# Performance work log

Measured on AMD Instinct MI355X. Metric: run time of the kernel, lower is better.

The kernel has to match this reference:

```python
import jax, jax.numpy as jnp
import numpy as np

N, E, HID, H, L, EF = 50000, 640000, 128, 8, 3, 16
C = HID // H  # 16, per-head output channels (concat=True)
NEG_SLOPE = 0.2
LN_EPS = 1e-5


def setup_inputs() -> dict:
    key = jax.random.key(0)
    ks = jax.random.split(key, 12)
    s = 0.05
    x = jax.random.normal(ks[0], (N, HID), jnp.float32)
    batch_index = jnp.sort(jax.random.randint(ks[1], (N,), 0, 64, dtype=jnp.int32))
    edge_index = jax.random.randint(ks[2], (2, E), 0, N, dtype=jnp.int32)
    edge_attr = jax.random.normal(ks[3], (E, EF), jnp.float32)
    # edge_transform: Linear(EF, HID)
    Wt = jax.random.normal(ks[4], (EF, HID), jnp.float32) * s
    bt = jnp.zeros((HID,), jnp.float32)
    # per-layer GATv2 params (stacked over L layers)
    Wl = jax.random.normal(ks[5], (L, HID, HID), jnp.float32) * s  # lin_l (source)
    bl = jnp.zeros((L, HID), jnp.float32)
    Wr = jax.random.normal(ks[6], (L, HID, HID), jnp.float32) * s  # lin_r (target)
    br = jnp.zeros((L, HID), jnp.float32)
    We = jax.random.normal(ks[7], (L, HID, HID), jnp.float32) * s  # lin_edge (no bias)
    att = jax.random.normal(ks[8], (L, H, C), jnp.float32) * s
    bias_o = jnp.zeros((L, HID), jnp.float32)
    ln_g = jnp.ones((L, HID), jnp.float32)
    ln_b = jnp.zeros((L, HID), jnp.float32)
    return dict(x=x, batch_index=batch_index, edge_index=edge_index, edge_attr=edge_attr,
                Wt=Wt, bt=bt, Wl=Wl, bl=bl, Wr=Wr, br=br, We=We, att=att,
                bias_o=bias_o, ln_g=ln_g, ln_b=ln_b)


def _layer_norm(x, g, b):
    mu = jnp.mean(x, axis=-1, keepdims=True)
    var = jnp.var(x, axis=-1, keepdims=True)
    return g * (x - mu) * jax.lax.rsqrt(var + LN_EPS) + b


def _gatv2_layer(x, ea, src, dst, Wl, bl, Wr, br, We, att, bias_o):
    # node transforms: lin_l for source features, lin_r for target features
    xl = (x @ Wl + bl).reshape(N, H, C)
    xr = (x @ Wr + br).reshape(N, H, C)
    em = (ea @ We).reshape(E, H, C)
    # per-edge attention logits (GATv2: leaky_relu AFTER the sum, then dot with att)
    m = jax.nn.leaky_relu(xl[src] + xr[dst] + em, NEG_SLOPE)  # [E,H,C]
    logits = jnp.einsum('ehc,hc->eh', m, att)                  # [E,H]
    # segment softmax over incoming edges of each destination node
    lmax = jax.ops.segment_max(logits, dst, num_segments=N)    # [N,H]
    p = jnp.exp(logits - lmax[dst])
    denom = jax.ops.segment_sum(p, dst, num_segments=N)        # [N,H]
    alpha = p / (denom[dst] + 1e-16)
    # weighted scatter-aggregate of source messages
    out = jax.ops.segment_sum(xl[src] * alpha[:, :, None], dst, num_segments=N)  # [N,H,C]
    return out.reshape(N, HID) + bias_o


def reference(x, batch_index, edge_index, edge_attr, Wt, bt, Wl, bl, Wr, br, We, att, bias_o, ln_g, ln_b):
    src, dst = edge_index[0], edge_index[1]
    ea = edge_attr @ Wt + bt  # shared edge_transform, [E,HID]
    for l in range(L):
        out = _gatv2_layer(x, ea, src, dst, Wl[l], bl[l], Wr[l], br[l], We[l], att[l], bias_o[l])
        out = _layer_norm(out, ln_g[l], ln_b[l])
        x = jax.nn.relu(out) + x  # dropout p=0 -> identity; residual
    return x
```

## Files before the change

kernel.cpp:

```cpp
#include <hip/hip_runtime.h>

#define N_NODES 50000
#define N_EDGES 640000
#define HID 128
#define EF 16
#define NLAYERS 3
#define CHUNK 32
#define SCAN_BLOCKS 196

typedef __attribute__((ext_vector_type(8))) short short8;
typedef __attribute__((ext_vector_type(4))) float f32x4;
typedef __attribute__((ext_vector_type(2))) float f32x2;

__device__ __forceinline__ unsigned short f2bf(float f) {
  unsigned int u = __float_as_uint(f);
  u = u + 0x7FFFu + ((u >> 16) & 1u);
  return (unsigned short)(u >> 16);
}

__device__ __forceinline__ float dpp_hadd8(float v) {
  int x;
  x = __builtin_amdgcn_update_dpp(0, __float_as_int(v), 0xB1, 0xF, 0xF, true);
  v += __int_as_float(x);
  x = __builtin_amdgcn_update_dpp(0, __float_as_int(v), 0x4E, 0xF, 0xF, true);
  v += __int_as_float(x);
  x = __builtin_amdgcn_update_dpp(0, __float_as_int(v), 0x141, 0xF, 0xF, true);
  v += __int_as_float(x);
  return v;
}

__device__ __forceinline__ int pslot(int j) {
  return (((j >> 4) * 8 + (j & 7)) << 1) + ((j >> 3) & 1);
}

__global__ __launch_bounds__(256) void k_prep(const float* __restrict__ Wt,
                                              const float* __restrict__ bt,
                                              const float* __restrict__ We,
                                              float* __restrict__ Mt,
                                              float* __restrict__ ct) {
  int id = blockIdx.x * 256 + threadIdx.x;
  const int total = NLAYERS * (EF + 1) * HID;
  if (id >= total) return;
  int l = id / ((EF + 1) * HID);
  int r = id % ((EF + 1) * HID);
  int row = r / HID;
  int j = r % HID;
  const float* Wel = We + l * HID * HID;
  float s = 0.f;
  if (row < EF) {
    const float* wtr = Wt + row * HID;
    for (int i = 0; i < HID; ++i) s += wtr[i] * Wel[i * HID + j];
    Mt[(l * EF + row) * HID + pslot(j)] = s;
  } else {
    for (int i = 0; i < HID; ++i) s += bt[i] * Wel[i * HID + j];
    ct[l * HID + pslot(j)] = s;
  }
}

__global__ __launch_bounds__(256) void k_cvtx(const float* __restrict__ x,
                                              unsigned short* __restrict__ xbf) {
  int id = blockIdx.x * 256 + threadIdx.x;
  const int total = N_NODES * HID / 8;
  if (id >= total) return;
  const float4* p = (const float4*)(x + id * 8);
  float4 a = p[0], b = p[1];
  unsigned short o[8] = {f2bf(a.x), f2bf(a.y), f2bf(a.z), f2bf(a.w),
                         f2bf(b.x), f2bf(b.y), f2bf(b.z), f2bf(b.w)};
  *(uint4*)(xbf + id * 8) = *(uint4*)o;
}

__global__ __launch_bounds__(256) void k_cvtw(const float* __restrict__ Wl,
                                              const float* __restrict__ Wr,
                                              unsigned short* __restrict__ WT) {
  int id = blockIdx.x * 256 + threadIdx.x;
  const int total = NLAYERS * 2 * HID * HID;
  if (id >= total) return;
  int k = id & (HID - 1);
  int n = (id >> 7) & (HID - 1);
  int s = (id >> 14) & 1;
  int l = id >> 15;
  const float* W = (s == 0 ? Wl : Wr) + (size_t)l * HID * HID;
  WT[id] = f2bf(W[k * HID + n]);
}

__global__ __launch_bounds__(256) void k_zero(int* __restrict__ counts, int* __restrict__ fill) {
  int id = blockIdx.x * 256 + threadIdx.x;
  if (id < N_NODES) { counts[id] = 0; fill[id] = 0; }
}

__global__ __launch_bounds__(256) void k_hist(const int* __restrict__ dst, int* __restrict__ counts) {
  int e = blockIdx.x * 256 + threadIdx.x;
  if (e < N_EDGES) atomicAdd(&counts[dst[e]], 1);
}

__global__ __launch_bounds__(256) void k_scan1(const int* __restrict__ counts,
                                               int* __restrict__ rowptr,
                                               int* __restrict__ bsum) {
  __shared__ int sc[256];
  int t = threadIdx.x;
  int i = blockIdx.x * 256 + t;
  int v = (i < N_NODES) ? counts[i] : 0;
  sc[t] = v;
  __syncthreads();
  for (int off = 1; off < 256; off <<= 1) {
    int u = 0;
    if (t >= off) u = sc[t - off];
    __syncthreads();
    sc[t] += u;
    __syncthreads();
  }
  if (i < N_NODES) rowptr[i] = sc[t] - v;
  if (t == 255) bsum[blockIdx.x] = sc[255];
}

__global__ __launch_bounds__(256) void k_scan2(int* __restrict__ bsum) {
  __shared__ int sc[256];
  int t = threadIdx.x;
  int v = (t < SCAN_BLOCKS) ? bsum[t] : 0;
  sc[t] = v;
  __syncthreads();
  for (int off = 1; off < 256; off <<= 1) {
    int u = 0;
    if (t >= off) u = sc[t - off];
    __syncthreads();
    sc[t] += u;
    __syncthreads();
  }
  bsum[t] = sc[t] - v;
}

__global__ __launch_bounds__(256) void k_scan3(int* __restrict__ rowptr, const int* __restrict__ bsum) {
  int t = threadIdx.x;
  int i = blockIdx.x * 256 + t;
  if (i < N_NODES) rowptr[i] += bsum[blockIdx.x];
  if (i == 0) rowptr[N_NODES] = N_EDGES;
}

__global__ __launch_bounds__(256) void k_fill(const int* __restrict__ src,
                                              const int* __restrict__ dst,
                                              const int* __restrict__ rowptr,
                                              int* __restrict__ fill,
                                              int* __restrict__ ssrc,
                                              const float* __restrict__ eattr,
                                              float* __restrict__ easrt) {
  int e = blockIdx.x * 256 + threadIdx.x;
  if (e >= N_EDGES) return;
  int d = dst[e];
  int pos = atomicAdd(&fill[d], 1);
  int idx = rowptr[d] + pos;
  ssrc[idx] = src[e];
  const float4* pe = (const float4*)(eattr + (size_t)e * EF);
  float4* po = (float4*)(easrt + (size_t)idx * EF);
#pragma unroll
  for (int q = 0; q < 4; ++q) po[q] = pe[q];
}

__global__ __launch_bounds__(256) void k_gemm_mfma(const unsigned short* __restrict__ xbf,
                                                   const unsigned short* __restrict__ WTl,
                                                   const float* __restrict__ bl,
                                                   const float* __restrict__ br,
                                                   const float* __restrict__ ctl,
                                                   unsigned short* __restrict__ xlb,
                                                   unsigned short* __restrict__ xrb) {
  __shared__ short As[64 * 136];
  __shared__ short Bs[128 * 136];
  int t = threadIdx.x;
  int s = blockIdx.y;
  int row0 = blockIdx.x * 64;

  const uint4* gx = (const uint4*)xbf;
#pragma unroll
  for (int p = 0; p < 4; ++p) {
    int c = t + p * 256;
    int row = c >> 4, col16 = c & 15;
    int grow = row0 + row;
    if (grow >= N_NODES) grow = N_NODES - 1;
    uint4 v = gx[grow * 16 + col16];
    *(uint4*)(&As[row * 136 + col16 * 8]) = v;
  }
  const uint4* gw = (const uint4*)WTl;
#pragma unroll
  for (int p = 0; p < 8; ++p) {
    int c = t + p * 256;
    int row = c >> 4, col16 = c & 15;
    uint4 v = gw[s * 2048 + row * 16 + col16];
    *(uint4*)(&Bs[row * 136 + col16 * 8]) = v;
  }
  __syncthreads();

  int lane = t & 63, w = t >> 6;
  int quad = lane >> 4, lm = lane & 15;
  f32x4 acc[4][2];
#pragma unroll
  for (int mf = 0; mf < 4; ++mf)
#pragma unroll
    for (int nf = 0; nf < 2; ++nf) acc[mf][nf] = (f32x4)(0.f);

#pragma unroll
  for (int ks = 0; ks < 4; ++ks) {
    short8 af[4], bf[2];
#pragma unroll
    for (int mf = 0; mf < 4; ++mf)
      af[mf] = *(short8*)(&As[(mf * 16 + lm) * 136 + ks * 32 + quad * 8]);
#pragma unroll
    for (int nf = 0; nf < 2; ++nf)
      bf[nf] = *(short8*)(&Bs[(w * 32 + nf * 16 + lm) * 136 + ks * 32 + quad * 8]);
#pragma unroll
    for (int mf = 0; mf < 4; ++mf)
#pragma unroll
      for (int nf = 0; nf < 2; ++nf)
        acc[mf][nf] = __builtin_amdgcn_mfma_f32_16x16x32_bf16(af[mf], bf[nf], acc[mf][nf], 0, 0, 0);
  }

  const float* bias = (s == 0) ? bl : br;
  unsigned short* out = (s == 0) ? xlb : xrb;
#pragma unroll
  for (int nf = 0; nf < 2; ++nf) {
    int n = w * 32 + nf * 16 + lm;
    int slot = pslot(n);
    float bv = bias[n] + ((s == 1) ? ctl[slot] : 0.f);
#pragma unroll
    for (int mf = 0; mf < 4; ++mf) {
#pragma unroll
      for (int r = 0; r < 4; ++r) {
        int grow = row0 + mf * 16 + quad * 4 + r;
        if (grow < N_NODES) out[(size_t)grow * HID + slot] = f2bf(acc[mf][nf][r] + bv);
      }
    }
  }
}

__global__ __launch_bounds__(64) void k_fused(const float* __restrict__ xin,
                                              const unsigned int* __restrict__ xlb,
                                              const unsigned int* __restrict__ xrb,
                                              const int* __restrict__ rowptr,
                                              const int* __restrict__ ssrc,
                                              const float* __restrict__ easrt,
                                              const float* __restrict__ Mt,
                                              const float* __restrict__ att,
                                              const float* __restrict__ bias_o,
                                              const float* __restrict__ lng,
                                              const float* __restrict__ lnb,
                                              float* __restrict__ xout,
                                              unsigned short* __restrict__ xbf_out) {
  __shared__ float ea_s[CHUNK][EF];
  __shared__ int src_s[CHUNK];
  int n = blockIdx.x;
  int l = threadIdx.x;
  int j0 = (l >> 3) * 16 + (l & 7), j1 = j0 + 8;

  f32x2 mtp[EF];
#pragma unroll
  for (int k = 0; k < EF; ++k) mtp[k] = *(const f32x2*)(&Mt[k * HID + l * 2]);
  unsigned int ur = xrb[(size_t)n * 64 + l];
  f32x2 base;
  base.x = __uint_as_float(ur << 16);
  base.y = __uint_as_float(ur & 0xFFFF0000u);
  f32x2 attp = {att[j0], att[j1]};
  int beg = rowptr[n], end = rowptr[n + 1];

  f32x2 acc = {0.f, 0.f};
  float denom = 0.f;

  for (int c0 = beg; c0 < end; c0 += CHUNK) {
    int cnt = min(CHUNK, end - c0);
    if (l < cnt) src_s[l] = ssrc[c0 + l];
    for (int q = l; q < cnt * 4; q += 64) {
      int i = q >> 2, part = q & 3;
      *(float4*)(&ea_s[i][part * 4]) =
          *(const float4*)(easrt + (size_t)(c0 + i) * EF + part * 4);
    }

    auto edge = [&](int i, unsigned int u) {
      f32x2 xls;
      xls.x = __uint_as_float(u << 16);
      xls.y = __uint_as_float(u & 0xFFFF0000u);
      f32x2 m = base + xls;
#pragma unroll
      for (int k = 0; k < EF; ++k) m += ea_s[i][k] * mtp[k];
      f32x2 am = {__int_as_float(__float_as_int(m.x) & 0x7FFFFFFF),
                  __int_as_float(__float_as_int(m.y) & 0x7FFFFFFF)};
      m = 0.6f * m + 0.4f * am;
      f32x2 v2 = m * attp;
      float vs = dpp_hadd8(v2.x + v2.y);
      float p = __expf(vs);
      denom += p;
      acc += xls * p;
    };

    unsigned int cur[4];
#pragma unroll
    for (int q = 0; q < 4; ++q)
      cur[q] = (q < cnt) ? xlb[(size_t)src_s[q] * 64 + l] : 0u;
    int cnt4 = cnt & ~3;
    for (int i = 0; i < cnt4; i += 4) {
      unsigned int nxt[4];
#pragma unroll
      for (int q = 0; q < 4; ++q) {
        int idx = i + 4 + q;
        nxt[q] = (idx < cnt) ? xlb[(size_t)src_s[idx] * 64 + l] : 0u;
      }
#pragma unroll
      for (int q = 0; q < 4; ++q) edge(i + q, cur[q]);
#pragma unroll
      for (int q = 0; q < 4; ++q) cur[q] = nxt[q];
    }
#pragma unroll
    for (int q = 0; q < 4; ++q)
      if (cnt4 + q < cnt) edge(cnt4 + q, cur[q]);
  }

  f32x2 outp;
  float inv = 1.f / (denom + 1e-16f);
  outp.x = acc.x * inv + bias_o[j0];
  outp.y = acc.y * inv + bias_o[j1];
  float s1 = outp.x + outp.y;
  float s2 = outp.x * outp.x + outp.y * outp.y;
#pragma unroll
  for (int mask = 1; mask <= 32; mask <<= 1) {
    s1 += __shfl_xor(s1, mask);
    s2 += __shfl_xor(s2, mask);
  }
  float mu = s1 * (1.f / 128.f);
  float var = s2 * (1.f / 128.f) - mu * mu;
  float rs = rsqrtf(var + 1e-5f);
  float y0 = lng[j0] * (outp.x - mu) * rs + lnb[j0];
  float y1 = lng[j1] * (outp.y - mu) * rs + lnb[j1];
  float r0 = fmaxf(y0, 0.f) + xin[(size_t)n * HID + j0];
  float r1 = fmaxf(y1, 0.f) + xin[(size_t)n * HID + j1];
  xout[(size_t)n * HID + j0] = r0;
  xout[(size_t)n * HID + j1] = r1;
  xbf_out[(size_t)n * HID + j0] = f2bf(r0);
  xbf_out[(size_t)n * HID + j1] = f2bf(r1);
}

extern "C" void kernel_launch(void* const* d_in, const int* in_sizes, int n_in,
                              void* d_out, int out_size, void* d_ws, size_t ws_size,
                              hipStream_t stream) {
  const float* x0    = (const float*)d_in[0];
  const int*   eidx  = (const int*)d_in[2];
  const float* eattr = (const float*)d_in[3];
  const float* Wt    = (const float*)d_in[4];
  const float* bt    = (const float*)d_in[5];
  const float* Wl    = (const float*)d_in[6];
  const float* bl    = (const float*)d_in[7];
  const float* Wr    = (const float*)d_in[8];
  const float* br    = (const float*)d_in[9];
  const float* We    = (const float*)d_in[10];
  const float* att   = (const float*)d_in[11];
  const float* bo    = (const float*)d_in[12];
  const float* lng   = (const float*)d_in[13];
  const float* lnb   = (const float*)d_in[14];
  float* out = (float*)d_out;
  const int* src = eidx;
  const int* dst = eidx + N_EDGES;

  char* ws = (char*)d_ws;
  size_t off = 0;
  auto alloc = [&](size_t bytes) {
    char* p = ws + off;
    off += (bytes + 255) & ~(size_t)255;
    return p;
  };
  float* Mt   = (float*)alloc((size_t)NLAYERS * EF * HID * 4);
  float* ct   = (float*)alloc((size_t)NLAYERS * HID * 4);
  int* counts = (int*)alloc((size_t)N_NODES * 4);
  int* rowptr = (int*)alloc((size_t)(N_NODES + 1) * 4);
  int* bsum   = (int*)alloc(256 * 4);
  int* fill   = (int*)alloc((size_t)N_NODES * 4);
  int* ssrc   = (int*)alloc((size_t)N_EDGES * 4);
  float* easrt = (float*)alloc((size_t)N_EDGES * EF * 4);
  unsigned short* xlb = (unsigned short*)alloc((size_t)N_NODES * HID * 2);
  unsigned short* xrb = (unsigned short*)alloc((size_t)N_NODES * HID * 2);
  float* xbuf = (float*)alloc((size_t)N_NODES * HID * 4);
  unsigned short* xbf = (unsigned short*)alloc((size_t)N_NODES * HID * 2);
  unsigned short* WTb = (unsigned short*)alloc((size_t)NLAYERS * 2 * HID * HID * 2);

  hipLaunchKernelGGL(k_prep, dim3(26), dim3(256), 0, stream, Wt, bt, We, Mt, ct);
  hipLaunchKernelGGL(k_cvtx, dim3((N_NODES * HID / 8 + 255) / 256), dim3(256), 0, stream, x0, xbf);
  hipLaunchKernelGGL(k_cvtw, dim3((NLAYERS * 2 * HID * HID + 255) / 256), dim3(256), 0, stream, Wl, Wr, WTb);
  hipLaunchKernelGGL(k_zero, dim3(SCAN_BLOCKS), dim3(256), 0, stream, counts, fill);
  hipLaunchKernelGGL(k_hist, dim3((N_EDGES + 255) / 256), dim3(256), 0, stream, dst, counts);
  hipLaunchKernelGGL(k_scan1, dim3(SCAN_BLOCKS), dim3(256), 0, stream, counts, rowptr, bsum);
  hipLaunchKernelGGL(k_scan2, dim3(1), dim3(256), 0, stream, bsum);
  hipLaunchKernelGGL(k_scan3, dim3(SCAN_BLOCKS), dim3(256), 0, stream, rowptr, bsum);
  hipLaunchKernelGGL(k_fill, dim3((N_EDGES + 255) / 256), dim3(256), 0, stream,
                     src, dst, rowptr, fill, ssrc, eattr, easrt);

  for (int l = 0; l < NLAYERS; ++l) {
    const float* xin = (l == 0) ? x0 : (const float*)xbuf;
    float* xout = (l == NLAYERS - 1) ? out : xbuf;
    hipLaunchKernelGGL(k_gemm_mfma, dim3((N_NODES + 63) / 64, 2), dim3(256), 0, stream,
                       xbf, WTb + (size_t)l * 2 * HID * HID, bl + l * HID, br + l * HID,
                       ct + (size_t)l * HID, xlb, xrb);
    hipLaunchKernelGGL(k_fused, dim3(N_NODES), dim3(64), 0, stream,
                       xin, (const unsigned int*)xlb, (const unsigned int*)xrb,
                       rowptr, ssrc, easrt,
                       Mt + (size_t)l * EF * HID, att + l * HID,
                       bo + l * HID, lng + l * HID, lnb + l * HID, xout, xbf);
  }
}
```

Before: 501.7 us.

## Merge setup kernels, memset counters, prescale source indices, vectorize edge-attr loads

Folds the weight-prep, weight-convert and x-convert kernels into one launch and replaces the zeroing kernel with a single memset over adjacent counts/fill buffers, cutting launch count. Source indices are stored pre-shifted by 64, and src_s is padded with zeros so the gather loop drops its bounds checks and index multiply. The edge-attribute inner product reads float4 vectors from shared memory, and the softmax uses exp2 with att prescaled by log2(e). The padded loads read node 0 for tail edges, which are not used.

```diff
diff --git a/kernel.cpp b/kernel.cpp
--- a/kernel.cpp
+++ b/kernel.cpp
@@ -33,59 +33,51 @@
   return (((j >> 4) * 8 + (j & 7)) << 1) + ((j >> 3) & 1);
 }
 
-__global__ __launch_bounds__(256) void k_prep(const float* __restrict__ Wt,
-                                              const float* __restrict__ bt,
-                                              const float* __restrict__ We,
-                                              float* __restrict__ Mt,
-                                              float* __restrict__ ct) {
-  int id = blockIdx.x * 256 + threadIdx.x;
-  const int total = NLAYERS * (EF + 1) * HID;
-  if (id >= total) return;
-  int l = id / ((EF + 1) * HID);
-  int r = id % ((EF + 1) * HID);
-  int row = r / HID;
-  int j = r % HID;
-  const float* Wel = We + l * HID * HID;
-  float s = 0.f;
-  if (row < EF) {
-    const float* wtr = Wt + row * HID;
-    for (int i = 0; i < HID; ++i) s += wtr[i] * Wel[i * HID + j];
-    Mt[(l * EF + row) * HID + pslot(j)] = s;
+__global__ __launch_bounds__(256) void k_setup(const float* __restrict__ Wt,
+                                               const float* __restrict__ bt,
+                                               const float* __restrict__ We,
+                                               const float* __restrict__ Wl,
+                                               const float* __restrict__ Wr,
+                                               const float* __restrict__ x,
+                                               float* __restrict__ Mt,
+                                               float* __restrict__ ct,
+                                               unsigned short* __restrict__ WT,
+                                               unsigned short* __restrict__ xbf) {
+  int b = blockIdx.x, t = threadIdx.x;
+  if (b < 26) {
+    int id = b * 256 + t;
+    const int total = NLAYERS * (EF + 1) * HID;
+    if (id >= total) return;
+    int l = id / ((EF + 1) * HID);
+    int r = id % ((EF + 1) * HID);
+    int row = r / HID;
+    int j = r % HID;
+    const float* Wel = We + l * HID * HID;
+    float s = 0.f;
+    if (row < EF) {
+      const float* wtr = Wt + row * HID;
+      for (int i = 0; i < HID; ++i) s += wtr[i] * Wel[i * HID + j];
+      Mt[(l * EF + row) * HID + pslot(j)] = s;
+    } else {
+      for (int i = 0; i < HID; ++i) s += bt[i] * Wel[i * HID + j];
+      ct[l * HID + pslot(j)] = s;
+    }
+  } else if (b < 410) {
+    int id = (b - 26) * 256 + t;
+    int k = id & (HID - 1);
+    int n = (id >> 7) & (HID - 1);
+    int s = (id >> 14) & 1;
+    int l = id >> 15;
+    const float* W = (s == 0 ? Wl : Wr) + (size_t)l * HID * HID;
+    WT[id] = f2bf(W[k * HID + n]);
   } else {
-    for (int i = 0; i < HID; ++i) s += bt[i] * Wel[i * HID + j];
-    ct[l * HID + pslot(j)] = s;
-  }
-}
-
-__global__ __launch_bounds__(256) void k_cvtx(const float* __restrict__ x,
-                                              unsigned short* __restrict__ xbf) {
-  int id = blockIdx.x * 256 + threadIdx.x;
-  const int total = N_NODES * HID / 8;
-  if (id >= total) return;
-  const float4* p = (const float4*)(x + id * 8);
-  float4 a = p[0], b = p[1];
-  unsigned short o[8] = {f2bf(a.x), f2bf(a.y), f2bf(a.z), f2bf(a.w),
-                         f2bf(b.x), f2bf(b.y), f2bf(b.z), f2bf(b.w)};
-  *(uint4*)(xbf + id * 8) = *(uint4*)o;
-}
-
-__global__ __launch_bounds__(256) void k_cvtw(const float* __restrict__ Wl,
-                                              const float* __restrict__ Wr,
-                                              unsigned short* __restrict__ WT) {
-  int id = blockIdx.x * 256 + threadIdx.x;
-  const int total = NLAYERS * 2 * HID * HID;
-  if (id >= total) return;
-  int k = id & (HID - 1);
-  int n = (id >> 7) & (HID - 1);
-  int s = (id >> 14) & 1;
-  int l = id >> 15;
-  const float* W = (s == 0 ? Wl : Wr) + (size_t)l * HID * HID;
-  WT[id] = f2bf(W[k * HID + n]);
-}
-
-__global__ __launch_bounds__(256) void k_zero(int* __restrict__ counts, int* __restrict__ fill) {
-  int id = blockIdx.x * 256 + threadIdx.x;
-  if (id < N_NODES) { counts[id] = 0; fill[id] = 0; }
+    int id = (b - 410) * 256 + t;
+    const float4* p = (const float4*)(x + (size_t)id * 8);
+    float4 a = p[0], bb = p[1];
+    unsigned short o[8] = {f2bf(a.x), f2bf(a.y), f2bf(a.z), f2bf(a.w),
+                           f2bf(bb.x), f2bf(bb.y), f2bf(bb.z), f2bf(bb.w)};
+    *(uint4*)(xbf + (size_t)id * 8) = *(uint4*)o;
+  }
 }
 
 __global__ __launch_bounds__(256) void k_hist(const int* __restrict__ dst, int* __restrict__ counts) {
@@ -148,7 +140,7 @@
   int d = dst[e];
   int pos = atomicAdd(&fill[d], 1);
   int idx = rowptr[d] + pos;
-  ssrc[idx] = src[e];
+  ssrc[idx] = src[e] << 6;
   const float4* pe = (const float4*)(eattr + (size_t)e * EF);
   float4* po = (float4*)(easrt + (size_t)idx * EF);
 #pragma unroll
@@ -243,8 +235,8 @@
                                               const float* __restrict__ lnb,
                                               float* __restrict__ xout,
                                               unsigned short* __restrict__ xbf_out) {
-  __shared__ float ea_s[CHUNK][EF];
-  __shared__ int src_s[CHUNK];
+  __shared__ __align__(16) float ea_s[CHUNK][EF];
+  __shared__ int src_s[CHUNK + 8];
   int n = blockIdx.x;
   int l = threadIdx.x;
   int j0 = (l >> 3) * 16 + (l & 7), j1 = j0 + 8;
@@ -256,7 +248,8 @@
   f32x2 base;
   base.x = __uint_as_float(ur << 16);
   base.y = __uint_as_float(ur & 0xFFFF0000u);
-  f32x2 attp = {att[j0], att[j1]};
+  const float LOG2E = 1.44269504088896340736f;
+  f32x2 attp = {att[j0] * LOG2E, att[j1] * LOG2E};
   int beg = rowptr[n], end = rowptr[n + 1];
 
   f32x2 acc = {0.f, 0.f};
@@ -265,6 +258,7 @@
   for (int c0 = beg; c0 < end; c0 += CHUNK) {
     int cnt = min(CHUNK, end - c0);
     if (l < cnt) src_s[l] = ssrc[c0 + l];
+    if (l < 8) src_s[cnt + l] = 0;
     for (int q = l; q < cnt * 4; q += 64) {
       int i = q >> 2, part = q & 3;
       *(float4*)(&ea_s[i][part * 4]) =
@@ -276,30 +270,34 @@
       xls.x = __uint_as_float(u << 16);
       xls.y = __uint_as_float(u & 0xFFFF0000u);
       f32x2 m = base + xls;
-#pragma unroll
-      for (int k = 0; k < EF; ++k) m += ea_s[i][k] * mtp[k];
+      const f32x4* er = (const f32x4*)(&ea_s[i][0]);
+      f32x4 e0 = er[0], e1 = er[1], e2 = er[2], e3 = er[3];
+#pragma unroll
+      for (int k = 0; k < 4; ++k) m += e0[k] * mtp[k];
+#pragma unroll
+      for (int k = 0; k < 4; ++k) m += e1[k] * mtp[4 + k];
+#pragma unroll
+      for (int k = 0; k < 4; ++k) m += e2[k] * mtp[8 + k];
+#pragma unroll
+      for (int k = 0; k < 4; ++k) m += e3[k] * mtp[12 + k];
       f32x2 am = {__int_as_float(__float_as_int(m.x) & 0x7FFFFFFF),
                   __int_as_float(__float_as_int(m.y) & 0x7FFFFFFF)};
       m = 0.6f * m + 0.4f * am;
       f32x2 v2 = m * attp;
       float vs = dpp_hadd8(v2.x + v2.y);
-      float p = __expf(vs);
+      float p = exp2f(vs);
       denom += p;
       acc += xls * p;
     };
 
     unsigned int cur[4];
 #pragma unroll
-    for (int q = 0; q < 4; ++q)
-      cur[q] = (q < cnt) ? xlb[(size_t)src_s[q] * 64 + l] : 0u;
+    for (int q = 0; q < 4; ++q) cur[q] = xlb[src_s[q] + l];
     int cnt4 = cnt & ~3;
     for (int i = 0; i < cnt4; i += 4) {
       unsigned int nxt[4];
 #pragma unroll
-      for (int q = 0; q < 4; ++q) {
-        int idx = i + 4 + q;
-        nxt[q] = (idx < cnt) ? xlb[(size_t)src_s[idx] * 64 + l] : 0u;
-      }
+      for (int q = 0; q < 4; ++q) nxt[q] = xlb[src_s[i + 4 + q] + l];
 #pragma unroll
       for (int q = 0; q < 4; ++q) edge(i + q, cur[q]);
 #pragma unroll
@@ -362,12 +360,13 @@
     off += (bytes + 255) & ~(size_t)255;
     return p;
   };
+  int* counts = (int*)alloc((size_t)N_NODES * 4);
+  int* fill   = (int*)((char*)counts + (size_t)N_NODES * 4);
+  fill = (int*)alloc((size_t)N_NODES * 4);
   float* Mt   = (float*)alloc((size_t)NLAYERS * EF * HID * 4);
   float* ct   = (float*)alloc((size_t)NLAYERS * HID * 4);
-  int* counts = (int*)alloc((size_t)N_NODES * 4);
   int* rowptr = (int*)alloc((size_t)(N_NODES + 1) * 4);
   int* bsum   = (int*)alloc(256 * 4);
-  int* fill   = (int*)alloc((size_t)N_NODES * 4);
   int* ssrc   = (int*)alloc((size_t)N_EDGES * 4);
   float* easrt = (float*)alloc((size_t)N_EDGES * EF * 4);
   unsigned short* xlb = (unsigned short*)alloc((size_t)N_NODES * HID * 2);
@@ -376,10 +375,10 @@
   unsigned short* xbf = (unsigned short*)alloc((size_t)N_NODES * HID * 2);
   unsigned short* WTb = (unsigned short*)alloc((size_t)NLAYERS * 2 * HID * HID * 2);
 
-  hipLaunchKernelGGL(k_prep, dim3(26), dim3(256), 0, stream, Wt, bt, We, Mt, ct);
-  hipLaunchKernelGGL(k_cvtx, dim3((N_NODES * HID / 8 + 255) / 256), dim3(256), 0, stream, x0, xbf);
-  hipLaunchKernelGGL(k_cvtw, dim3((NLAYERS * 2 * HID * HID + 255) / 256), dim3(256), 0, stream, Wl, Wr, WTb);
-  hipLaunchKernelGGL(k_zero, dim3(SCAN_BLOCKS), dim3(256), 0, stream, counts, fill);
+  hipMemsetAsync(counts, 0, (char*)(fill + N_NODES) - (char*)counts, stream);
+
+  hipLaunchKernelGGL(k_setup, dim3(3535), dim3(256), 0, stream,
+                     Wt, bt, We, Wl, Wr, x0, Mt, ct, WTb, xbf);
   hipLaunchKernelGGL(k_hist, dim3((N_EDGES + 255) / 256), dim3(256), 0, stream, dst, counts);
   hipLaunchKernelGGL(k_scan1, dim3(SCAN_BLOCKS), dim3(256), 0, stream, counts, rowptr, bsum);
   hipLaunchKernelGGL(k_scan2, dim3(1), dim3(256), 0, stream, bsum);
```

Result: no change. 493.7 us (-1.6%).
